# Optimization experiments

Measured on AMD Instinct MI355X. Metric: run time of the kernel, lower is better.

The kernel has to match this reference:

```python
import jax, jax.numpy as jnp
import numpy as np

N = 50000   # nodes
E = 800000  # edges
D = 128     # att_dim
H = 8       # heads
DH = D // H # head dim
EPS = 1e-5


def _ln(x, g, b):
    m = jnp.mean(x, axis=-1, keepdims=True)
    v = jnp.mean((x - m) ** 2, axis=-1, keepdims=True)
    return (x - m) * jax.lax.rsqrt(v + EPS) * g + b


def setup_inputs() -> dict:
    key = jax.random.key(0)
    ks = jax.random.split(key, 12)
    s = 1.0 / np.sqrt(D)
    w = lambda k, sh: (jax.random.normal(k, sh, jnp.float32) * s)
    return {
        'x': jax.random.normal(ks[0], (N, D), jnp.float32),
        'idx_i': jax.random.randint(ks[1], (E,), 0, N, jnp.int32),
        'idx_j': jax.random.randint(ks[2], (E,), 0, N, jnp.int32),
        'Wq': w(ks[3], (D, D)), 'bq': jnp.zeros((D,), jnp.float32),
        'Wk': w(ks[4], (D, D)), 'bk': jnp.zeros((D,), jnp.float32),
        'Wv': w(ks[5], (D, D)), 'bv': jnp.zeros((D,), jnp.float32),
        'Wo': w(ks[6], (D, D)), 'bo': jnp.zeros((D,), jnp.float32),
        'g1': jnp.ones((D,), jnp.float32), 'be1': jnp.zeros((D,), jnp.float32),
        'W1': w(ks[7], (D, D)), 'bb1': jnp.zeros((D,), jnp.float32),
        'W2': w(ks[8], (D, D)), 'bb2': jnp.zeros((D,), jnp.float32),
        'g2': jnp.ones((D,), jnp.float32), 'be2': jnp.zeros((D,), jnp.float32),
    }


def reference(x, idx_i, idx_j, Wq, bq, Wk, bk, Wv, bv, Wo, bo,
              g1, be1, W1, bb1, W2, bb2, g2, be2):
    # --- EdgeAttentionLayer: multi-head dot-product attention over edges ---
    q = (x @ Wq + bq).reshape(N, H, DH)   # n h d
    k = (x @ Wk + bk).reshape(N, H, DH)
    v = (x @ Wv + bv).reshape(N, H, DH)
    q_i = q[idx_i]                         # (E, H, DH) gather at destination
    k_j = k[idx_j]                         # (E, H, DH) gather at source
    e = jnp.einsum('ehd,ehd->eh', q_i, k_j) / np.sqrt(DH)  # (E, H)
    # segment softmax over edges sharing the same destination node idx_i
    m = jax.ops.segment_max(e, idx_i, num_segments=N)       # (N, H)
    a = jnp.exp(e - m[idx_i])
    denom = jax.ops.segment_sum(a, idx_i, num_segments=N)   # (N, H)
    alpha = a / denom[idx_i]                                 # (E, H)
    agg = jax.ops.segment_sum(alpha[:, :, None] * v[idx_j], idx_i,
                              num_segments=N)                # (N, H, DH)
    x1 = agg.reshape(N, D) @ Wo + bo
    # --- residual + LayerNorm ---
    h = _ln(x + x1, g1, be1)
    # --- ResLayer projection: Linear -> ReLU -> Linear, residual, LayerNorm ---
    y = jax.nn.relu(h @ W1 + bb1) @ W2 + bb2
    return _ln(h + y, g2, be2)
```

## Files before the change

kernel.cpp:

```cpp
#include <hip/hip_runtime.h>
#include <hip/hip_bf16.h>
#include <math.h>

#define D 128
#define H 8
#define DH 16
#define SCAN_CHUNK 1024

typedef __attribute__((ext_vector_type(8))) short bf16x8;
typedef __attribute__((ext_vector_type(4))) float f32x4;

__device__ __forceinline__ float bf2f(ushort u) {
    unsigned int x = ((unsigned int)u) << 16;
    float f;
    __builtin_memcpy(&f, &x, 4);
    return f;
}
__device__ __forceinline__ ushort f2bf(float f) {
    __hip_bfloat16 h = __float2bfloat16(f);
    ushort u;
    __builtin_memcpy(&u, &h, 2);
    return u;
}

__device__ __forceinline__ void load_split8(const float* src, bf16x8* hi, bf16x8* lo) {
    float4 a = *(const float4*)src;
    float4 b = *(const float4*)(src + 4);
    float xs[8] = {a.x, a.y, a.z, a.w, b.x, b.y, b.z, b.w};
    short hv[8], lv[8];
    #pragma unroll
    for (int i = 0; i < 8; ++i) {
        ushort hb = f2bf(xs[i]);
        hv[i] = (short)hb;
        lv[i] = (short)f2bf(xs[i] - bf2f(hb));
    }
    *hi = (bf16x8){hv[0], hv[1], hv[2], hv[3], hv[4], hv[5], hv[6], hv[7]};
    *lo = (bf16x8){lv[0], lv[1], lv[2], lv[3], lv[4], lv[5], lv[6], lv[7]};
}

#define STAGE_W(SRC, LDSBUF)                                              \
    {                                                                      \
        _Pragma("unroll")                                                  \
        for (int it_ = 0; it_ < 8; ++it_) {                                \
            int idx16_ = t + it_ * 256;                                    \
            int row_ = idx16_ >> 4, c16_ = idx16_ & 15;                    \
            int d_ = (row_ << 7) + ((c16_ ^ (row_ & 7)) << 3);             \
            *(bf16x8*)((LDSBUF) + d_) = *(const bf16x8*)((SRC) + idx16_ * 8); \
        }                                                                  \
    }

#define LOAD_A(SRCH, SRCL, BASE, AH, AL)                                   \
    _Pragma("unroll")                                                      \
    for (int kk_ = 0; kk_ < 4; ++kk_) {                                    \
        AH[kk_] = *(const bf16x8*)((SRCH) + (BASE) + kk_ * 32);            \
        AL[kk_] = *(const bf16x8*)((SRCL) + (BASE) + kk_ * 32);            \
    }

#define TILE_MFMA(AH0, AL0, AH1, AL1, WH, ACC0, ACC1)                      \
    _Pragma("unroll")                                                      \
    for (int kk = 0; kk < 4; ++kk) {                                       \
        _Pragma("unroll")                                                  \
        for (int n = 0; n < 8; ++n) {                                      \
            int rn = n * 16 + l15;                                         \
            int off = (rn << 7) + (((l4 + kk * 4) ^ (rn & 7)) << 3);       \
            bf16x8 bh = *(const bf16x8*)((WH) + off);                      \
            ACC0[n] = __builtin_amdgcn_mfma_f32_16x16x32_bf16(AH0[kk], bh, ACC0[n], 0, 0, 0); \
            ACC0[n] = __builtin_amdgcn_mfma_f32_16x16x32_bf16(AL0[kk], bh, ACC0[n], 0, 0, 0); \
            ACC1[n] = __builtin_amdgcn_mfma_f32_16x16x32_bf16(AH1[kk], bh, ACC1[n], 0, 0, 0); \
            ACC1[n] = __builtin_amdgcn_mfma_f32_16x16x32_bf16(AL1[kk], bh, ACC1[n], 0, 0, 0); \
        }                                                                  \
    }


__global__ __launch_bounds__(256) void prep_w_kernel(
    const float* __restrict__ w0, const float* __restrict__ w1,
    const float* __restrict__ w2, const float* __restrict__ w3,
    const float* __restrict__ w4, const float* __restrict__ w5,
    ushort* __restrict__ wth, int* __restrict__ count, int n_nodes)
{
    __shared__ __align__(16) float tile[128][132];
    const int m = blockIdx.x;
    const float* W = (m == 0) ? w0 : (m == 1) ? w1 : (m == 2) ? w2
                   : (m == 3) ? w3 : (m == 4) ? w4 : w5;
    const int t = threadIdx.x;
    for (int idx = m * 256 + t; idx < n_nodes; idx += 6 * 256) count[idx] = 0;

    const float4* wg = (const float4*)W;
    #pragma unroll
    for (int it = 0; it < 16; ++it) {
        int f4 = t + it * 256;
        int k = f4 >> 5, c4 = f4 & 31;
        *((float4*)&tile[k][c4 * 4]) = wg[f4];
    }
    __syncthreads();
    ushort* oh = wth + m * 16384;
    #pragma unroll
    for (int it = 0; it < 64; ++it) {
        int idx = t + it * 256;
        int c = idx >> 7, k = idx & 127;
        oh[idx] = f2bf(tile[k][c]);
    }
}


__global__ __launch_bounds__(256) void gemm_qkv_kernel(
    const float* __restrict__ x,
    const ushort* __restrict__ wth,
    const float* __restrict__ bq, const float* __restrict__ bk,
    const float* __restrict__ bv,
    const int* __restrict__ idx_i, int* __restrict__ count, int n_edges,
    float* __restrict__ q, ushort* __restrict__ k16, ushort* __restrict__ v16,
    int n_rows)
{
    __shared__ __align__(16) ushort wh[16384];
    const int t = threadIdx.x;
    const int w = t >> 6, l = t & 63;
    const int l15 = l & 15, l4 = l >> 4;
    const int m = blockIdx.y;

    STAGE_W(wth + m * 16384, wh);

    if (m == 0) {
        const int stride = gridDim.x * 256;
        for (int e = blockIdx.x * 256 + t; e < n_edges; e += stride)
            atomicAdd(&count[idx_i[e]], 1);
    }

    const float* bias = (m == 0) ? bq : (m == 1) ? bk : bv;
    float bsv[8];
    #pragma unroll
    for (int n = 0; n < 8; ++n) bsv[n] = bias[n * 16 + l15];
    __syncthreads();

    const int ntiles = (n_rows + 127) >> 7;
    for (int tile = blockIdx.x; tile < ntiles; tile += gridDim.x) {
        const int rowb = tile * 128 + w * 32;
        const size_t a0 = (size_t)(rowb + l15) * D + l4 * 8;
        bf16x8 ah0[4], al0[4], ah1[4], al1[4];
        #pragma unroll
        for (int kk = 0; kk < 4; ++kk) {
            load_split8(x + a0 + kk * 32, &ah0[kk], &al0[kk]);
            load_split8(x + a0 + 16 * D + kk * 32, &ah1[kk], &al1[kk]);
        }
        f32x4 acc0[8], acc1[8];
        #pragma unroll
        for (int n = 0; n < 8; ++n) {
            acc0[n] = (f32x4){0.f, 0.f, 0.f, 0.f};
            acc1[n] = (f32x4){0.f, 0.f, 0.f, 0.f};
        }
        TILE_MFMA(ah0, al0, ah1, al1, wh, acc0, acc1);
        #pragma unroll
        for (int n = 0; n < 8; ++n) {
            int col = n * 16 + l15;
            #pragma unroll
            for (int r = 0; r < 4; ++r) {
                int row0 = rowb + l4 * 4 + r;
                int row1 = row0 + 16;
                if (row0 < n_rows) {
                    float val = acc0[n][r] + bsv[n];
                    if (m == 0) q[(size_t)row0 * D + col] = val;
                    else if (m == 1) k16[(size_t)row0 * D + col] = f2bf(val);
                    else v16[(size_t)row0 * D + col] = f2bf(val);
                }
                if (row1 < n_rows) {
                    float val = acc1[n][r] + bsv[n];
                    if (m == 0) q[(size_t)row1 * D + col] = val;
                    else if (m == 1) k16[(size_t)row1 * D + col] = f2bf(val);
                    else v16[(size_t)row1 * D + col] = f2bf(val);
                }
            }
        }
    }
}


__global__ __launch_bounds__(256) void scan_reduce_kernel(
    const int* __restrict__ count, int* __restrict__ bsum, int n)
{
    __shared__ int wsum[4];
    const int t = threadIdx.x, lane = t & 63, w = t >> 6;
    int base = blockIdx.x * SCAN_CHUNK + t * 4;
    int s = 0;
    #pragma unroll
    for (int i = 0; i < 4; ++i) {
        int idx = base + i;
        if (idx < n) s += count[idx];
    }
    #pragma unroll
    for (int off = 1; off < 64; off <<= 1) s += __shfl_xor(s, off);
    if (lane == 0) wsum[w] = s;
    __syncthreads();
    if (t == 0) bsum[blockIdx.x] = wsum[0] + wsum[1] + wsum[2] + wsum[3];
}


__global__ __launch_bounds__(256) void scan_write_kernel(
    const int* __restrict__ count, const int* __restrict__ bsum,
    int* __restrict__ row_start, int* __restrict__ cursor, int nb, int n)
{
    __shared__ int wtot[4];
    __shared__ int base_sh;
    const int t = threadIdx.x, lane = t & 63, w = t >> 6;
    if (w == 0) {
        int v = (lane < nb) ? bsum[lane] : 0;
        int pre = (lane < (int)blockIdx.x) ? v : 0;
        #pragma unroll
        for (int off = 1; off < 64; off <<= 1) pre += __shfl_xor(pre, off);
        if (lane == 0) base_sh = pre;
        if (blockIdx.x == 0) {
            int tot = v;
            #pragma unroll
            for (int off = 1; off < 64; off <<= 1) tot += __shfl_xor(tot, off);
            if (lane == 0) row_start[n] = tot;
        }
    }
    int base = blockIdx.x * SCAN_CHUNK + t * 4;
    int c0 = 0, c1 = 0, c2 = 0, c3 = 0;
    if (base + 0 < n) c0 = count[base + 0];
    if (base + 1 < n) c1 = count[base + 1];
    if (base + 2 < n) c2 = count[base + 2];
    if (base + 3 < n) c3 = count[base + 3];
    int tsum = c0 + c1 + c2 + c3;
    int inc = tsum;
    #pragma unroll
    for (int off = 1; off < 64; off <<= 1) {
        int u = __shfl_up(inc, off);
        if (lane >= off) inc += u;
    }
    if (lane == 63) wtot[w] = inc;
    __syncthreads();
    int wb = 0;
    for (int i = 0; i < w; ++i) wb += wtot[i];
    int start = base_sh + wb + inc - tsum;
    if (base + 0 < n) { row_start[base + 0] = start;            cursor[base + 0] = start; }
    if (base + 1 < n) { row_start[base + 1] = start + c0;       cursor[base + 1] = start + c0; }
    if (base + 2 < n) { row_start[base + 2] = start + c0 + c1;  cursor[base + 2] = start + c0 + c1; }
    if (base + 3 < n) { row_start[base + 3] = start + c0 + c1 + c2; cursor[base + 3] = start + c0 + c1 + c2; }
}

__global__ __launch_bounds__(256) void scatter_kernel(
    const int* __restrict__ idx_i, const int* __restrict__ idx_j,
    int* __restrict__ cursor, int* __restrict__ ejs, int n_edges)
{
    int e = blockIdx.x * blockDim.x + threadIdx.x;
    if (e < n_edges) {
        int i = idx_i[e];
        int pos = atomicAdd(&cursor[i], 1);
        ejs[pos] = idx_j[e];
    }
}


__global__ __launch_bounds__(256) void fused_agg_kernel(
    const float* __restrict__ q, const ushort* __restrict__ k16,
    const ushort* __restrict__ v16, const int* __restrict__ row_start,
    const int* __restrict__ ejs,
    ushort* __restrict__ aggh, ushort* __restrict__ aggl, int n_nodes)
{
    const int lane = threadIdx.x & 63;
    const int node = (blockIdx.x * blockDim.x + threadIdx.x) >> 6;
    if (node >= n_nodes) return;
    const int beg = row_start[node], end = row_start[node + 1];
    const int half = lane >> 5, sl = lane & 31;
    const int c4 = sl * 4;

    if (beg >= end) {
        if (half == 0) {
            ((uint2*)(aggh + (size_t)node * D))[sl] = make_uint2(0u, 0u);
            ((uint2*)(aggl + (size_t)node * D))[sl] = make_uint2(0u, 0u);
        }
        return;
    }

    const float SC = 0.25f * 1.4426950408889634f;
    float4 qv = *(const float4*)&q[(size_t)node * D + c4];
    qv.x *= SC; qv.y *= SC; qv.z *= SC; qv.w *= SC;
    float m = -INFINITY, l = 0.f;
    float a0 = 0.f, a1 = 0.f, a2 = 0.f, a3 = 0.f;

    int p = beg + half;
    uint2 kr0, vr0, kr1, vr1;
    if (p < end) {
        int j = ejs[p];
        kr0 = *(const uint2*)(k16 + (size_t)j * D + c4);
        vr0 = *(const uint2*)(v16 + (size_t)j * D + c4);
    }
    if (p + 2 < end) {
        int j = ejs[p + 2];
        kr1 = *(const uint2*)(k16 + (size_t)j * D + c4);
        vr1 = *(const uint2*)(v16 + (size_t)j * D + c4);
    }
    while (p < end) {
        uint2 kc = kr0, vc = vr0;
        kr0 = kr1; vr0 = vr1;
        if (p + 4 < end) {
            int j = ejs[p + 4];
            kr1 = *(const uint2*)(k16 + (size_t)j * D + c4);
            vr1 = *(const uint2*)(v16 + (size_t)j * D + c4);
        }
        float k0 = bf2f((ushort)kc.x), k1 = bf2f((ushort)(kc.x >> 16));
        float k2 = bf2f((ushort)kc.y), k3 = bf2f((ushort)(kc.y >> 16));
        float s = qv.x * k0 + qv.y * k1 + qv.z * k2 + qv.w * k3;
        s += __shfl_xor(s, 1);
        s += __shfl_xor(s, 2);
        float v0 = bf2f((ushort)vc.x), v1 = bf2f((ushort)(vc.x >> 16));
        float v2 = bf2f((ushort)vc.y), v3 = bf2f((ushort)(vc.y >> 16));
        if (__any(s > m + 8.f)) {
            float mn = fmaxf(m, s);
            float c  = exp2f(m - mn);
            float pe = exp2f(s - mn);
            l  = l  * c + pe;
            a0 = a0 * c + pe * v0;
            a1 = a1 * c + pe * v1;
            a2 = a2 * c + pe * v2;
            a3 = a3 * c + pe * v3;
            m = mn;
        } else {
            float pe = exp2f(s - m);
            l += pe;
            a0 = fmaf(pe, v0, a0);
            a1 = fmaf(pe, v1, a1);
            a2 = fmaf(pe, v2, a2);
            a3 = fmaf(pe, v3, a3);
        }
        p += 2;
    }

    float m2 = __shfl_xor(m, 32);
    float l2 = __shfl_xor(l, 32);
    float b0 = __shfl_xor(a0, 32);
    float b1 = __shfl_xor(a1, 32);
    float b2 = __shfl_xor(a2, 32);
    float b3 = __shfl_xor(a3, 32);
    float mm = fmaxf(m, m2);
    float cA = exp2f(m - mm);
    float cB = exp2f(m2 - mm);
    float L  = l * cA + l2 * cB;
    float A0 = a0 * cA + b0 * cB;
    float A1 = a1 * cA + b1 * cB;
    float A2 = a2 * cA + b2 * cB;
    float A3 = a3 * cA + b3 * cB;
    float invl = (L > 0.f) ? (1.0f / L) : 0.f;
    float o0 = A0 * invl, o1 = A1 * invl, o2 = A2 * invl, o3 = A3 * invl;

    ushort h0 = f2bf(o0), h1 = f2bf(o1), h2 = f2bf(o2), h3 = f2bf(o3);
    if (half == 0) {
        uint2 hv;
        hv.x = (unsigned int)h0 | ((unsigned int)h1 << 16);
        hv.y = (unsigned int)h2 | ((unsigned int)h3 << 16);
        ((uint2*)(aggh + (size_t)node * D))[sl] = hv;
    } else {
        ushort l0 = f2bf(o0 - bf2f(h0)), l1 = f2bf(o1 - bf2f(h1));
        ushort l2_ = f2bf(o2 - bf2f(h2)), l3 = f2bf(o3 - bf2f(h3));
        uint2 lv;
        lv.x = (unsigned int)l0 | ((unsigned int)l1 << 16);
        lv.y = (unsigned int)l2_ | ((unsigned int)l3 << 16);
        ((uint2*)(aggl + (size_t)node * D))[sl] = lv;
    }
}


__global__ __launch_bounds__(256) void gemm_oproj_kernel(
    const ushort* __restrict__ aggh, const ushort* __restrict__ aggl,
    const float* __restrict__ x,
    const ushort* __restrict__ wth,
    const float* __restrict__ bo, const float* __restrict__ g1,
    const float* __restrict__ be1,
    ushort* __restrict__ hh, ushort* __restrict__ hl, int n_rows)
{
    __shared__ __align__(16) ushort wh[16384];
    const int t = threadIdx.x;
    const int w = t >> 6, l = t & 63;
    const int l15 = l & 15, l4 = l >> 4;

    STAGE_W(wth, wh);
    float bsv[8], gv[8], bev[8];
    #pragma unroll
    for (int n = 0; n < 8; ++n) {
        int col = n * 16 + l15;
        bsv[n] = bo[col]; gv[n] = g1[col]; bev[n] = be1[col];
    }
    __syncthreads();

    const int ntiles = (n_rows + 127) >> 7;
    for (int tile = blockIdx.x; tile < ntiles; tile += gridDim.x) {
        const int rowb = tile * 128 + w * 32;
        const size_t a0 = (size_t)(rowb + l15) * D + l4 * 8;
        bf16x8 ah0[4], al0[4], ah1[4], al1[4];
        LOAD_A(aggh, aggl, a0, ah0, al0);
        LOAD_A(aggh, aggl, a0 + 16 * D, ah1, al1);
        f32x4 acc0[8], acc1[8];
        #pragma unroll
        for (int n = 0; n < 8; ++n) {
            acc0[n] = (f32x4){0.f, 0.f, 0.f, 0.f};
            acc1[n] = (f32x4){0.f, 0.f, 0.f, 0.f};
        }
        TILE_MFMA(ah0, al0, ah1, al1, wh, acc0, acc1);
        #pragma unroll
        for (int g = 0; g < 2; ++g) {
            f32x4* acc = g ? acc1 : acc0;
            int rbase = rowb + g * 16;
            float vals[8][4];
            #pragma unroll
            for (int n = 0; n < 8; ++n) {
                int col = n * 16 + l15;
                #pragma unroll
                for (int r = 0; r < 4; ++r) {
                    int row = rbase + l4 * 4 + r;
                    float xr = (row < n_rows) ? x[(size_t)row * D + col] : 0.f;
                    vals[n][r] = acc[n][r] + bsv[n] + xr;
                }
            }
            #pragma unroll
            for (int r = 0; r < 4; ++r) {
                int row = rbase + l4 * 4 + r;
                float s = 0.f, ss = 0.f;
                #pragma unroll
                for (int n = 0; n < 8; ++n) { s += vals[n][r]; ss += vals[n][r] * vals[n][r]; }
                #pragma unroll
                for (int msk = 1; msk <= 8; msk <<= 1) {
                    s += __shfl_xor(s, msk);
                    ss += __shfl_xor(ss, msk);
                }
                float mean = s * (1.0f / D);
                float var = ss * (1.0f / D) - mean * mean;
                float inv = rsqrtf(var + 1e-5f);
                if (row < n_rows) {
                    #pragma unroll
                    for (int n = 0; n < 8; ++n) {
                        int col = n * 16 + l15;
                        float y = (vals[n][r] - mean) * inv * gv[n] + bev[n];
                        ushort hb = f2bf(y);
                        hh[(size_t)row * D + col] = hb;
                        hl[(size_t)row * D + col] = f2bf(y - bf2f(hb));
                    }
                }
            }
        }
    }
}


__global__ __launch_bounds__(256) void gemm_ffn1_kernel(
    const ushort* __restrict__ hh, const ushort* __restrict__ hl,
    const ushort* __restrict__ wth,
    const float* __restrict__ bb1,
    ushort* __restrict__ th, ushort* __restrict__ tl, int n_rows)
{
    __shared__ __align__(16) ushort wh[16384];
    const int t = threadIdx.x;
    const int w = t >> 6, l = t & 63;
    const int l15 = l & 15, l4 = l >> 4;

    STAGE_W(wth, wh);
    float bsv[8];
    #pragma unroll
    for (int n = 0; n < 8; ++n) bsv[n] = bb1[n * 16 + l15];
    __syncthreads();

    const int ntiles = (n_rows + 127) >> 7;
    for (int tile = blockIdx.x; tile < ntiles; tile += gridDim.x) {
        const int rowb = tile * 128 + w * 32;
        const size_t a0 = (size_t)(rowb + l15) * D + l4 * 8;
        bf16x8 ah0[4], al0[4], ah1[4], al1[4];
        LOAD_A(hh, hl, a0, ah0, al0);
        LOAD_A(hh, hl, a0 + 16 * D, ah1, al1);
        f32x4 acc0[8], acc1[8];
        #pragma unroll
        for (int n = 0; n < 8; ++n) {
            acc0[n] = (f32x4){0.f, 0.f, 0.f, 0.f};
            acc1[n] = (f32x4){0.f, 0.f, 0.f, 0.f};
        }
        TILE_MFMA(ah0, al0, ah1, al1, wh, acc0, acc1);
        #pragma unroll
        for (int n = 0; n < 8; ++n) {
            int col = n * 16 + l15;
            #pragma unroll
            for (int r = 0; r < 4; ++r) {
                int row0 = rowb + l4 * 4 + r;
                int row1 = row0 + 16;
                if (row0 < n_rows) {
                    float tv = fmaxf(acc0[n][r] + bsv[n], 0.f);
                    ushort hb = f2bf(tv);
                    th[(size_t)row0 * D + col] = hb;
                    tl[(size_t)row0 * D + col] = f2bf(tv - bf2f(hb));
                }
                if (row1 < n_rows) {
                    float tv = fmaxf(acc1[n][r] + bsv[n], 0.f);
                    ushort hb = f2bf(tv);
                    th[(size_t)row1 * D + col] = hb;
                    tl[(size_t)row1 * D + col] = f2bf(tv - bf2f(hb));
                }
            }
        }
    }
}


__global__ __launch_bounds__(256) void gemm_ffn2_kernel(
    const ushort* __restrict__ th, const ushort* __restrict__ tl,
    const ushort* __restrict__ hh, const ushort* __restrict__ hl,
    const ushort* __restrict__ wth,
    const float* __restrict__ bb2, const float* __restrict__ g2,
    const float* __restrict__ be2,
    float* __restrict__ out, int n_rows)
{
    __shared__ __align__(16) ushort wh[16384];
    const int t = threadIdx.x;
    const int w = t >> 6, l = t & 63;
    const int l15 = l & 15, l4 = l >> 4;

    STAGE_W(wth, wh);
    float bsv[8], gv[8], bev[8];
    #pragma unroll
    for (int n = 0; n < 8; ++n) {
        int col = n * 16 + l15;
        bsv[n] = bb2[col]; gv[n] = g2[col]; bev[n] = be2[col];
    }
    __syncthreads();

    const int ntiles = (n_rows + 127) >> 7;
    for (int tile = blockIdx.x; tile < ntiles; tile += gridDim.x) {
        const int rowb = tile * 128 + w * 32;
        const size_t a0 = (size_t)(rowb + l15) * D + l4 * 8;
        bf16x8 ah0[4], al0[4], ah1[4], al1[4];
        LOAD_A(th, tl, a0, ah0, al0);
        LOAD_A(th, tl, a0 + 16 * D, ah1, al1);
        f32x4 acc0[8], acc1[8];
        #pragma unroll
        for (int n = 0; n < 8; ++n) {
            acc0[n] = (f32x4){0.f, 0.f, 0.f, 0.f};
            acc1[n] = (f32x4){0.f, 0.f, 0.f, 0.f};
        }
        TILE_MFMA(ah0, al0, ah1, al1, wh, acc0, acc1);
        #pragma unroll
        for (int g = 0; g < 2; ++g) {
            f32x4* acc = g ? acc1 : acc0;
            int rbase = rowb + g * 16;
            float vals[8][4];
            #pragma unroll
            for (int n = 0; n < 8; ++n) {
                int col = n * 16 + l15;
                #pragma unroll
                for (int r = 0; r < 4; ++r) {
                    int row = rbase + l4 * 4 + r;
                    float hr = 0.f;
                    if (row < n_rows)
                        hr = bf2f(hh[(size_t)row * D + col]) + bf2f(hl[(size_t)row * D + col]);
                    vals[n][r] = acc[n][r] + bsv[n] + hr;
                }
            }
            #pragma unroll
            for (int r = 0; r < 4; ++r) {
                int row = rbase + l4 * 4 + r;
                float s = 0.f, ss = 0.f;
                #pragma unroll
                for (int n = 0; n < 8; ++n) { s += vals[n][r]; ss += vals[n][r] * vals[n][r]; }
                #pragma unroll
                for (int msk = 1; msk <= 8; msk <<= 1) {
                    s += __shfl_xor(s, msk);
                    ss += __shfl_xor(ss, msk);
                }
                float mean = s * (1.0f / D);
                float var = ss * (1.0f / D) - mean * mean;
                float inv = rsqrtf(var + 1e-5f);
                if (row < n_rows) {
                    #pragma unroll
                    for (int n = 0; n < 8; ++n) {
                        int col = n * 16 + l15;
                        out[(size_t)row * D + col] = (vals[n][r] - mean) * inv * gv[n] + bev[n];
                    }
                }
            }
        }
    }
}


extern "C" void kernel_launch(void* const* d_in, const int* in_sizes, int n_in,
                              void* d_out, int out_size, void* d_ws, size_t ws_size,
                              hipStream_t stream) {
    const float* x     = (const float*)d_in[0];
    const int*   idx_i = (const int*)d_in[1];
    const int*   idx_j = (const int*)d_in[2];
    const float* Wq = (const float*)d_in[3];
    const float* bq = (const float*)d_in[4];
    const float* Wk = (const float*)d_in[5];
    const float* bk = (const float*)d_in[6];
    const float* Wv = (const float*)d_in[7];
    const float* bv = (const float*)d_in[8];
    const float* Wo = (const float*)d_in[9];
    const float* bo = (const float*)d_in[10];
    const float* g1 = (const float*)d_in[11];
    const float* be1 = (const float*)d_in[12];
    const float* W1 = (const float*)d_in[13];
    const float* bb1 = (const float*)d_in[14];
    const float* W2 = (const float*)d_in[15];
    const float* bb2 = (const float*)d_in[16];
    const float* g2 = (const float*)d_in[17];
    const float* be2 = (const float*)d_in[18];

    const int N_ = in_sizes[0] / D;
    const int E_ = in_sizes[1];
    const size_t ND = (size_t)N_ * D;
    const int nb = (N_ + SCAN_CHUNK - 1) / SCAN_CHUNK;
    const int ntiles = (N_ + 127) >> 7;

    float* ws = (float*)d_ws;
    float* q = ws;
    ushort* k16 = (ushort*)(q + ND);
    ushort* v16 = k16 + ND;
    int* count     = (int*)(v16 + ND);
    int* row_start = count + N_;
    int* cursor    = row_start + N_ + 1;
    int* bsum      = cursor + N_;
    int* ejs       = bsum + 64;
    ushort* aggh = (ushort*)(ejs + E_);
    ushort* aggl = aggh + ND;
    ushort* wth = aggl + ND;
    ushort* hh = (ushort*)q;
    ushort* hl = hh + ND;
    ushort* th = k16;
    ushort* tl = v16;

    prep_w_kernel<<<6, 256, 0, stream>>>(Wq, Wk, Wv, Wo, W1, W2, wth, count, N_);
    {
        dim3 g(ntiles, 3);
        gemm_qkv_kernel<<<g, 256, 0, stream>>>(x, wth, bq, bk, bv,
                                               idx_i, count, E_,
                                               q, k16, v16, N_);
    }
    scan_reduce_kernel<<<nb, 256, 0, stream>>>(count, bsum, N_);
    scan_write_kernel<<<nb, 256, 0, stream>>>(count, bsum, row_start, cursor, nb, N_);
    scatter_kernel<<<(E_ + 255) / 256, 256, 0, stream>>>(idx_i, idx_j, cursor, ejs, E_);
    fused_agg_kernel<<<(N_ + 3) / 4, 256, 0, stream>>>(q, k16, v16, row_start, ejs,
                                                       aggh, aggl, N_);
    gemm_oproj_kernel<<<ntiles, 256, 0, stream>>>(aggh, aggl, x, wth + 3 * 16384,
                                                  bo, g1, be1, hh, hl, N_);
    gemm_ffn1_kernel<<<ntiles, 256, 0, stream>>>(hh, hl, wth + 4 * 16384,
                                                 bb1, th, tl, N_);
    gemm_ffn2_kernel<<<ntiles, 256, 0, stream>>>(th, tl, hh, hl, wth + 5 * 16384,
                                                 bb2, g2, be2, (float*)d_out, N_);
}
```

Measured before the change: 244.5 us.

## Store Q in bf16 and process four edges per wave with 16-byte loads

The QKV GEMM now writes Q as bf16 instead of fp32, halving Q store and load traffic. The edge-attention kernel splits each 64-lane wave into four 16-lane groups, each handling one edge with 8 channels per lane via uint4 loads. This gives four edges in flight per wave instead of two, and the prefetch distance rises accordingly. Per-group online-softmax states are merged with two xor-shuffle rounds. Rounding Q to bf16 adds some error to the attention logits, and each lane now holds more registers.

```diff
diff --git a/kernel.cpp b/kernel.cpp
--- a/kernel.cpp
+++ b/kernel.cpp
@@ -109,7 +109,7 @@
     const float* __restrict__ bq, const float* __restrict__ bk,
     const float* __restrict__ bv,
     const int* __restrict__ idx_i, int* __restrict__ count, int n_edges,
-    float* __restrict__ q, ushort* __restrict__ k16, ushort* __restrict__ v16,
+    ushort* __restrict__ qh, ushort* __restrict__ k16, ushort* __restrict__ v16,
     int n_rows)
 {
     __shared__ __align__(16) ushort wh[16384];
@@ -158,13 +158,13 @@
                 int row1 = row0 + 16;
                 if (row0 < n_rows) {
                     float val = acc0[n][r] + bsv[n];
-                    if (m == 0) q[(size_t)row0 * D + col] = val;
+                    if (m == 0) qh[(size_t)row0 * D + col] = f2bf(val);
                     else if (m == 1) k16[(size_t)row0 * D + col] = f2bf(val);
                     else v16[(size_t)row0 * D + col] = f2bf(val);
                 }
                 if (row1 < n_rows) {
                     float val = acc1[n][r] + bsv[n];
-                    if (m == 0) q[(size_t)row1 * D + col] = val;
+                    if (m == 0) qh[(size_t)row1 * D + col] = f2bf(val);
                     else if (m == 1) k16[(size_t)row1 * D + col] = f2bf(val);
                     else v16[(size_t)row1 * D + col] = f2bf(val);
                 }
@@ -252,7 +252,7 @@
 
 
 __global__ __launch_bounds__(256) void fused_agg_kernel(
-    const float* __restrict__ q, const ushort* __restrict__ k16,
+    const ushort* __restrict__ qh, const ushort* __restrict__ k16,
     const ushort* __restrict__ v16, const int* __restrict__ row_start,
     const int* __restrict__ ejs,
     ushort* __restrict__ aggh, ushort* __restrict__ aggl, int n_nodes)
@@ -261,101 +261,119 @@
     const int node = (blockIdx.x * blockDim.x + threadIdx.x) >> 6;
     if (node >= n_nodes) return;
     const int beg = row_start[node], end = row_start[node + 1];
-    const int half = lane >> 5, sl = lane & 31;
-    const int c4 = sl * 4;
+    const int grp = lane >> 4, sl = lane & 15;
+    const int c8 = sl * 8;
 
     if (beg >= end) {
-        if (half == 0) {
-            ((uint2*)(aggh + (size_t)node * D))[sl] = make_uint2(0u, 0u);
-            ((uint2*)(aggl + (size_t)node * D))[sl] = make_uint2(0u, 0u);
-        }
+        if (grp == 0) ((uint4*)(aggh + (size_t)node * D))[sl] = make_uint4(0u, 0u, 0u, 0u);
+        else if (grp == 1) ((uint4*)(aggl + (size_t)node * D))[sl] = make_uint4(0u, 0u, 0u, 0u);
         return;
     }
 
     const float SC = 0.25f * 1.4426950408889634f;
-    float4 qv = *(const float4*)&q[(size_t)node * D + c4];
-    qv.x *= SC; qv.y *= SC; qv.z *= SC; qv.w *= SC;
-    float m = -INFINITY, l = 0.f;
-    float a0 = 0.f, a1 = 0.f, a2 = 0.f, a3 = 0.f;
-
-    int p = beg + half;
-    uint2 kr0, vr0, kr1, vr1;
+    uint4 qw = *(const uint4*)(qh + (size_t)node * D + c8);
+    float qv[8];
+    qv[0] = bf2f((ushort)qw.x) * SC;  qv[1] = bf2f((ushort)(qw.x >> 16)) * SC;
+    qv[2] = bf2f((ushort)qw.y) * SC;  qv[3] = bf2f((ushort)(qw.y >> 16)) * SC;
+    qv[4] = bf2f((ushort)qw.z) * SC;  qv[5] = bf2f((ushort)(qw.z >> 16)) * SC;
+    qv[6] = bf2f((ushort)qw.w) * SC;  qv[7] = bf2f((ushort)(qw.w >> 16)) * SC;
+
+    float m = -1e30f, l = 0.f;
+    float a[8];
+    #pragma unroll
+    for (int i = 0; i < 8; ++i) a[i] = 0.f;
+
+    int p = beg + grp;
+    uint4 kr0, vr0, kr1, vr1;
     if (p < end) {
         int j = ejs[p];
-        kr0 = *(const uint2*)(k16 + (size_t)j * D + c4);
-        vr0 = *(const uint2*)(v16 + (size_t)j * D + c4);
-    }
-    if (p + 2 < end) {
-        int j = ejs[p + 2];
-        kr1 = *(const uint2*)(k16 + (size_t)j * D + c4);
-        vr1 = *(const uint2*)(v16 + (size_t)j * D + c4);
+        kr0 = *(const uint4*)(k16 + (size_t)j * D + c8);
+        vr0 = *(const uint4*)(v16 + (size_t)j * D + c8);
+    }
+    if (p + 4 < end) {
+        int j = ejs[p + 4];
+        kr1 = *(const uint4*)(k16 + (size_t)j * D + c8);
+        vr1 = *(const uint4*)(v16 + (size_t)j * D + c8);
     }
     while (p < end) {
-        uint2 kc = kr0, vc = vr0;
+        uint4 kc = kr0, vc = vr0;
         kr0 = kr1; vr0 = vr1;
-        if (p + 4 < end) {
-            int j = ejs[p + 4];
-            kr1 = *(const uint2*)(k16 + (size_t)j * D + c4);
-            vr1 = *(const uint2*)(v16 + (size_t)j * D + c4);
-        }
-        float k0 = bf2f((ushort)kc.x), k1 = bf2f((ushort)(kc.x >> 16));
-        float k2 = bf2f((ushort)kc.y), k3 = bf2f((ushort)(kc.y >> 16));
-        float s = qv.x * k0 + qv.y * k1 + qv.z * k2 + qv.w * k3;
+        if (p + 8 < end) {
+            int j = ejs[p + 8];
+            kr1 = *(const uint4*)(k16 + (size_t)j * D + c8);
+            vr1 = *(const uint4*)(v16 + (size_t)j * D + c8);
+        }
+        float kf[8];
+        kf[0] = bf2f((ushort)kc.x);  kf[1] = bf2f((ushort)(kc.x >> 16));
+        kf[2] = bf2f((ushort)kc.y);  kf[3] = bf2f((ushort)(kc.y >> 16));
+        kf[4] = bf2f((ushort)kc.z);  kf[5] = bf2f((ushort)(kc.z >> 16));
+        kf[6] = bf2f((ushort)kc.w);  kf[7] = bf2f((ushort)(kc.w >> 16));
+        float s = 0.f;
+        #pragma unroll
+        for (int i = 0; i < 8; ++i) s = fmaf(qv[i], kf[i], s);
         s += __shfl_xor(s, 1);
-        s += __shfl_xor(s, 2);
-        float v0 = bf2f((ushort)vc.x), v1 = bf2f((ushort)(vc.x >> 16));
-        float v2 = bf2f((ushort)vc.y), v3 = bf2f((ushort)(vc.y >> 16));
+        float vf[8];
+        vf[0] = bf2f((ushort)vc.x);  vf[1] = bf2f((ushort)(vc.x >> 16));
+        vf[2] = bf2f((ushort)vc.y);  vf[3] = bf2f((ushort)(vc.y >> 16));
+        vf[4] = bf2f((ushort)vc.z);  vf[5] = bf2f((ushort)(vc.z >> 16));
+        vf[6] = bf2f((ushort)vc.w);  vf[7] = bf2f((ushort)(vc.w >> 16));
         if (__any(s > m + 8.f)) {
             float mn = fmaxf(m, s);
             float c  = exp2f(m - mn);
             float pe = exp2f(s - mn);
-            l  = l  * c + pe;
-            a0 = a0 * c + pe * v0;
-            a1 = a1 * c + pe * v1;
-            a2 = a2 * c + pe * v2;
-            a3 = a3 * c + pe * v3;
+            l = l * c + pe;
+            #pragma unroll
+            for (int i = 0; i < 8; ++i) a[i] = a[i] * c + pe * vf[i];
             m = mn;
         } else {
             float pe = exp2f(s - m);
             l += pe;
-            a0 = fmaf(pe, v0, a0);
-            a1 = fmaf(pe, v1, a1);
-            a2 = fmaf(pe, v2, a2);
-            a3 = fmaf(pe, v3, a3);
-        }
-        p += 2;
-    }
-
-    float m2 = __shfl_xor(m, 32);
-    float l2 = __shfl_xor(l, 32);
-    float b0 = __shfl_xor(a0, 32);
-    float b1 = __shfl_xor(a1, 32);
-    float b2 = __shfl_xor(a2, 32);
-    float b3 = __shfl_xor(a3, 32);
-    float mm = fmaxf(m, m2);
-    float cA = exp2f(m - mm);
-    float cB = exp2f(m2 - mm);
-    float L  = l * cA + l2 * cB;
-    float A0 = a0 * cA + b0 * cB;
-    float A1 = a1 * cA + b1 * cB;
-    float A2 = a2 * cA + b2 * cB;
-    float A3 = a3 * cA + b3 * cB;
-    float invl = (L > 0.f) ? (1.0f / L) : 0.f;
-    float o0 = A0 * invl, o1 = A1 * invl, o2 = A2 * invl, o3 = A3 * invl;
-
-    ushort h0 = f2bf(o0), h1 = f2bf(o1), h2 = f2bf(o2), h3 = f2bf(o3);
-    if (half == 0) {
-        uint2 hv;
-        hv.x = (unsigned int)h0 | ((unsigned int)h1 << 16);
-        hv.y = (unsigned int)h2 | ((unsigned int)h3 << 16);
-        ((uint2*)(aggh + (size_t)node * D))[sl] = hv;
-    } else {
-        ushort l0 = f2bf(o0 - bf2f(h0)), l1 = f2bf(o1 - bf2f(h1));
-        ushort l2_ = f2bf(o2 - bf2f(h2)), l3 = f2bf(o3 - bf2f(h3));
-        uint2 lv;
-        lv.x = (unsigned int)l0 | ((unsigned int)l1 << 16);
-        lv.y = (unsigned int)l2_ | ((unsigned int)l3 << 16);
-        ((uint2*)(aggl + (size_t)node * D))[sl] = lv;
+            #pragma unroll
+            for (int i = 0; i < 8; ++i) a[i] = fmaf(pe, vf[i], a[i]);
+        }
+        p += 4;
+    }
+
+    #pragma unroll
+    for (int off = 16; off <= 32; off <<= 1) {
+        float m2 = __shfl_xor(m, off);
+        float l2 = __shfl_xor(l, off);
+        float b[8];
+        #pragma unroll
+        for (int i = 0; i < 8; ++i) b[i] = __shfl_xor(a[i], off);
+        float mm = fmaxf(m, m2);
+        float cA = exp2f(m - mm);
+        float cB = exp2f(m2 - mm);
+        l = l * cA + l2 * cB;
+        #pragma unroll
+        for (int i = 0; i < 8; ++i) a[i] = a[i] * cA + b[i] * cB;
+        m = mm;
+    }
+    float invl = (l > 0.f) ? (1.0f / l) : 0.f;
+    float o[8];
+    #pragma unroll
+    for (int i = 0; i < 8; ++i) o[i] = a[i] * invl;
+
+    ushort hb[8];
+    #pragma unroll
+    for (int i = 0; i < 8; ++i) hb[i] = f2bf(o[i]);
+    if (grp == 0) {
+        uint4 hv;
+        hv.x = (unsigned int)hb[0] | ((unsigned int)hb[1] << 16);
+        hv.y = (unsigned int)hb[2] | ((unsigned int)hb[3] << 16);
+        hv.z = (unsigned int)hb[4] | ((unsigned int)hb[5] << 16);
+        hv.w = (unsigned int)hb[6] | ((unsigned int)hb[7] << 16);
+        ((uint4*)(aggh + (size_t)node * D))[sl] = hv;
+    } else if (grp == 1) {
+        ushort lb[8];
+        #pragma unroll
+        for (int i = 0; i < 8; ++i) lb[i] = f2bf(o[i] - bf2f(hb[i]));
+        uint4 lv;
+        lv.x = (unsigned int)lb[0] | ((unsigned int)lb[1] << 16);
+        lv.y = (unsigned int)lb[2] | ((unsigned int)lb[3] << 16);
+        lv.z = (unsigned int)lb[4] | ((unsigned int)lb[5] << 16);
+        lv.w = (unsigned int)lb[6] | ((unsigned int)lb[7] << 16);
+        ((uint4*)(aggl + (size_t)node * D))[sl] = lv;
     }
 }
 
@@ -607,8 +625,8 @@
     const int ntiles = (N_ + 127) >> 7;
 
     float* ws = (float*)d_ws;
-    float* q = ws;
-    ushort* k16 = (ushort*)(q + ND);
+    float* qbuf = ws;
+    ushort* k16 = (ushort*)(qbuf + ND);
     ushort* v16 = k16 + ND;
     int* count     = (int*)(v16 + ND);
     int* row_start = count + N_;
@@ -618,7 +636,8 @@
     ushort* aggh = (ushort*)(ejs + E_);
     ushort* aggl = aggh + ND;
     ushort* wth = aggl + ND;
-    ushort* hh = (ushort*)q;
+    ushort* qh = (ushort*)qbuf;
+    ushort* hh = (ushort*)qbuf;
     ushort* hl = hh + ND;
     ushort* th = k16;
     ushort* tl = v16;
@@ -628,12 +647,12 @@
         dim3 g(ntiles, 3);
         gemm_qkv_kernel<<<g, 256, 0, stream>>>(x, wth, bq, bk, bv,
                                                idx_i, count, E_,
-                                               q, k16, v16, N_);
+                                               qh, k16, v16, N_);
     }
     scan_reduce_kernel<<<nb, 256, 0, stream>>>(count, bsum, N_);
     scan_write_kernel<<<nb, 256, 0, stream>>>(count, bsum, row_start, cursor, nb, N_);
     scatter_kernel<<<(E_ + 255) / 256, 256, 0, stream>>>(idx_i, idx_j, cursor, ejs, E_);
-    fused_agg_kernel<<<(N_ + 3) / 4, 256, 0, stream>>>(q, k16, v16, row_start, ejs,
+    fused_agg_kernel<<<(N_ + 3) / 4, 256, 0, stream>>>(qh, k16, v16, row_start, ejs,
                                                        aggh, aggl, N_);
     gemm_oproj_kernel<<<ntiles, 256, 0, stream>>>(aggh, aggl, x, wth + 3 * 16384,
                                                   bo, g1, be1, hh, hl, N_);
```

Result: no change. 244.4 us (-0.1%).
